# Performance work log

Measured on AMD Instinct MI355X. Metric: run time of the kernel, lower is better.

Reference implementation:

```python
import jax, jax.numpy as jnp
import numpy as np

N = 50000
IN_CH = 128
HEADS = 4
OUT_CH = 32
E = 800000
NEG_SLOPE = 0.2


def setup_inputs() -> dict:
    key = jax.random.key(0)
    k1, k2, k3, k4, k5, k6 = jax.random.split(key, 6)
    x = jax.random.normal(k1, (N, IN_CH), dtype=jnp.float32)
    edge_index = jax.random.randint(k2, (2, E), 0, N, dtype=jnp.int64)
    # learned params (PyG GATv2Conv: lin_l, lin_r weights, att vector, bias)
    s = 1.0 / np.sqrt(IN_CH)
    W_l = jax.random.uniform(k3, (IN_CH, HEADS, OUT_CH), jnp.float32, -s, s)
    W_r = jax.random.uniform(k4, (IN_CH, HEADS, OUT_CH), jnp.float32, -s, s)
    att = jax.random.uniform(k5, (HEADS, OUT_CH), jnp.float32, -s, s)
    bias = jax.random.uniform(k6, (HEADS * OUT_CH,), jnp.float32, -s, s)
    return {"x": x, "edge_index": edge_index, "W_l": W_l, "W_r": W_r,
            "att": att, "bias": bias}


def reference(x, edge_index, W_l, W_r, att, bias):
    # add self loops (PyG default add_self_loops=True)
    loops = jnp.arange(N, dtype=edge_index.dtype)
    src = jnp.concatenate([edge_index[0], loops])  # message source j
    dst = jnp.concatenate([edge_index[1], loops])  # message target i

    # node projections: [N, H, C]
    x_l = jnp.einsum('nd,dhc->nhc', x, W_l)  # source-side
    x_r = jnp.einsum('nd,dhc->nhc', x, W_r)  # target-side

    # GATv2 attention logits per edge: a^T LeakyReLU(x_l[j] + x_r[i])
    e = jax.nn.leaky_relu(x_l[src] + x_r[dst], NEG_SLOPE)  # [Etot, H, C]
    score = jnp.einsum('ehc,hc->eh', e, att)               # [Etot, H]

    # segment softmax over incoming edges of each destination node
    m = jax.ops.segment_max(score, dst, num_segments=N)    # [N, H]
    m = jnp.where(jnp.isfinite(m), m, 0.0)
    ex = jnp.exp(score - m[dst])                           # [Etot, H]
    denom = jax.ops.segment_sum(ex, dst, num_segments=N)   # [N, H]
    alpha = ex / denom[dst]                                # [Etot, H]

    # scatter-aggregate weighted messages
    msg = alpha[:, :, None] * x_l[src]                     # [Etot, H, C]
    out = jax.ops.segment_sum(msg, dst, num_segments=N)    # [N, H, C]

    # concat heads + bias
    return out.reshape(N, HEADS * OUT_CH) + bias
```

## Files before the change

kernel.cpp:

```cpp
#include <hip/hip_runtime.h>
#include <math.h>

#define N_NODES 50000
#define IN_CH   128
#define TOT_CH  128
#define NEDGE   800000
#define ETOT    (NEDGE + N_NODES)
#define MTILES  ((N_NODES + 63) / 64)
#define NBUCK   ((N_NODES + 255) / 256)
#define BCAP    8192
#define EPB     4096
#define NBIN    ((ETOT + EPB - 1) / EPB)

#define OFF_XL      ((size_t)0)
#define OFF_EBUF    ((size_t)12800000)
#define OFF_XR      ((size_t)25600000)
#define OFF_SRC     ((size_t)38400000)
#define OFF_BT      ((size_t)44900352)
#define OFF_GCUR    ((size_t)45000064)
#define OFF_ROWPTR  ((size_t)51200000)

typedef float f32x4 __attribute__((ext_vector_type(4)));
typedef short s16x8 __attribute__((ext_vector_type(8)));

__device__ __forceinline__ unsigned f2bf(float f) {
    unsigned u = __float_as_uint(f);
    return (u + 0x7fffu + ((u >> 16) & 1u)) >> 16;
}
__device__ __forceinline__ float bflo(unsigned u) { return __uint_as_float(u << 16); }
__device__ __forceinline__ float bfhi(unsigned u) { return __uint_as_float(u & 0xffff0000u); }

__device__ __forceinline__ int SWZ(int row, int byteoff) {
    return row * 256 + (byteoff ^ ((row & 7) << 4));
}

__global__ __launch_bounds__(256) void k1_kernel(
    const float* __restrict__ Wl, const float* __restrict__ Wr,
    unsigned* __restrict__ btg, const int* __restrict__ ei,
    int* __restrict__ gcur, unsigned* __restrict__ ebuf)
{
    __shared__ int lcnt[256];
    __shared__ int lbase[256];
    const int bid = blockIdx.x;
    const int tid = threadIdx.x;

    if (bid < NBIN) {
        lcnt[tid] = 0;
        __syncthreads();
        const int base = bid * EPB;
        int sv[16], dv[16];
#pragma unroll
        for (int u = 0; u < 16; ++u) {
            const int e = base + u * 256 + tid;
            int s32 = 0, d32 = -1;
            if (e < ETOT) {
                if (e < NEDGE) { s32 = ei[e]; d32 = ei[NEDGE + e]; }
                else           { s32 = d32 = e - NEDGE; }
                atomicAdd(&lcnt[d32 >> 8], 1);
            }
            sv[u] = s32; dv[u] = d32;
        }
        __syncthreads();
        if (tid < NBUCK) {
            const int v = lcnt[tid];
            lbase[tid] = v ? atomicAdd(&gcur[tid], v) : 0;
        }
        __syncthreads();
        lcnt[tid] = 0;
        __syncthreads();
#pragma unroll
        for (int u = 0; u < 16; ++u) {
            const int d32 = dv[u];
            if (d32 >= 0) {
                const int b = d32 >> 8;
                const int p = lbase[b] + atomicAdd(&lcnt[b], 1);
                ebuf[b * BCAP + p] = (unsigned)sv[u] | ((unsigned)(d32 & 255) << 16);
            }
        }
    } else {
        const int g = (bid - NBIN) * 256 + tid;
        if (g < 256 * 64) {
            const int n = g >> 6, kk = g & 63;
            const float* W = (n < 128) ? Wl : Wr;
            const int nc = n & 127;
            const float a = W[(size_t)(2 * kk) * 128 + nc];
            const float b = W[(size_t)(2 * kk + 1) * 128 + nc];
            btg[g] = f2bf(a) | (f2bf(b) << 16);
        }
    }
}

__global__ __launch_bounds__(256) void k2_kernel(
    const float* __restrict__ x, const unsigned* __restrict__ btg,
    unsigned* __restrict__ xl_bf, unsigned* __restrict__ xr_bf,
    const unsigned* __restrict__ ebuf, const int* __restrict__ gcur,
    int2* __restrict__ rowptr2, int* __restrict__ ssrc)
{
    __shared__ __align__(16) unsigned char smem[32768];
    __shared__ int wsum[4];
    const int bid = blockIdx.x;
    const int tid = threadIdx.x;

    if (bid < NBUCK) {
        int* lcnt = (int*)smem;
        int* lcur = ((int*)smem) + 256;
        const int ecnt  = gcur[bid];
        const int ebase = bid * BCAP;
        lcnt[tid] = 0;
        __syncthreads();
        for (int k = tid; k < ecnt; k += 256)
            atomicAdd(&lcnt[(ebuf[ebase + k] >> 16) & 255], 1);
        __syncthreads();
        const int lane = tid & 63, wid = tid >> 6;
        const int v = lcnt[tid];
        int s = v;
#pragma unroll
        for (int off = 1; off < 64; off <<= 1) {
            int t = __shfl_up(s, off);
            if (lane >= off) s += t;
        }
        if (lane == 63) wsum[wid] = s;
        __syncthreads();
        if (tid == 0) {
            int acc = 0;
#pragma unroll
            for (int w = 0; w < 4; ++w) { int t = wsum[w]; wsum[w] = acc; acc += t; }
        }
        __syncthreads();
        const int gpos = ebase + wsum[wid] + s - v;
        const int node = (bid << 8) + tid;
        if (node < N_NODES) rowptr2[node] = make_int2(gpos, gpos + v);
        lcur[tid] = gpos;
        __syncthreads();
        for (int k = tid; k < ecnt; k += 256) {
            const unsigned ed = ebuf[ebase + k];
            const int p = atomicAdd(&lcur[(ed >> 16) & 255], 1);
            ssrc[p] = (int)(ed & 0xffffu);
        }
        return;
    }

    unsigned char* Al = smem;
    unsigned char* Bl = smem + 16384;
    const int gb = bid - NBUCK;
    const int nt = gb / MTILES;
    const int mt = gb % MTILES;
    const int mbase = mt * 64;
    const int nbase = nt * 64;

    {
        const int r = tid >> 2, q = tid & 3;
        int gm = mbase + r;
        gm = (gm < N_NODES) ? gm : (N_NODES - 1);
        const float* xrow = x + (size_t)gm * IN_CH + q * 32;
#pragma unroll
        for (int i = 0; i < 8; ++i) {
            const float4 xv = *(const float4*)(xrow + i * 4);
            uint2 p;
            p.x = f2bf(xv.x) | (f2bf(xv.y) << 16);
            p.y = f2bf(xv.z) | (f2bf(xv.w) << 16);
            *(uint2*)(Al + SWZ(r, q * 64 + i * 8)) = p;
        }
    }
    {
        const int r = tid >> 2, q = tid & 3;
        const unsigned* brow = btg + (size_t)(nbase + r) * 64 + q * 16;
#pragma unroll
        for (int i = 0; i < 4; ++i) {
            const uint4 v = *(const uint4*)(brow + i * 4);
            *(uint4*)(Bl + SWZ(r, q * 64 + i * 16)) = v;
        }
    }
    __syncthreads();

    const int l  = tid & 63;
    const int wv = tid >> 6;

    f32x4 acc[4];
#pragma unroll
    for (int n = 0; n < 4; ++n) acc[n] = (f32x4){0.f, 0.f, 0.f, 0.f};

    s16x8 af[4];
#pragma unroll
    for (int ks = 0; ks < 4; ++ks)
        af[ks] = *(const s16x8*)(Al + SWZ(wv * 16 + (l & 15), ks * 64 + (l >> 4) * 16));

#pragma unroll
    for (int nsub = 0; nsub < 4; ++nsub) {
#pragma unroll
        for (int ks = 0; ks < 4; ++ks) {
            const s16x8 bfr = *(const s16x8*)(Bl + SWZ(nsub * 16 + (l & 15), ks * 64 + (l >> 4) * 16));
            acc[nsub] = __builtin_amdgcn_mfma_f32_16x16x32_bf16(af[ks], bfr, acc[nsub], 0, 0, 0);
        }
    }

    unsigned* dstbuf = (nt < 2) ? xl_bf : xr_bf;
    const int ncol0 = (nt & 1) * 64;
#pragma unroll
    for (int nsub = 0; nsub < 4; ++nsub) {
        const int n = ncol0 + nsub * 16 + (l & 15);
#pragma unroll
        for (int reg = 0; reg < 4; ++reg) {
            const float v  = acc[nsub][reg];
            const float vp = __shfl_xor(v, 1);
            const int row = mbase + wv * 16 + (l >> 4) * 4 + reg;
            if (((l & 1) == 0) && row < N_NODES)
                dstbuf[(size_t)row * 64 + (n >> 1)] = f2bf(v) | (f2bf(vp) << 16);
        }
    }
}

#define DPP_ADD(s, ctrl) do { \
        int _t = __builtin_amdgcn_update_dpp(0, __float_as_int(s), ctrl, 0xf, 0xf, true); \
        s += __int_as_float(_t); } while(0)

#define RED16x8(a0,a1,a2,a3,a4,a5,a6,a7) do { \
        DPP_ADD(a0,0xB1); DPP_ADD(a1,0xB1); DPP_ADD(a2,0xB1); DPP_ADD(a3,0xB1); \
        DPP_ADD(a4,0xB1); DPP_ADD(a5,0xB1); DPP_ADD(a6,0xB1); DPP_ADD(a7,0xB1); \
        DPP_ADD(a0,0x4E); DPP_ADD(a1,0x4E); DPP_ADD(a2,0x4E); DPP_ADD(a3,0x4E); \
        DPP_ADD(a4,0x4E); DPP_ADD(a5,0x4E); DPP_ADD(a6,0x4E); DPP_ADD(a7,0x4E); \
        DPP_ADD(a0,0x124); DPP_ADD(a1,0x124); DPP_ADD(a2,0x124); DPP_ADD(a3,0x124); \
        DPP_ADD(a4,0x124); DPP_ADD(a5,0x124); DPP_ADD(a6,0x124); DPP_ADD(a7,0x124); \
        DPP_ADD(a0,0x128); DPP_ADD(a1,0x128); DPP_ADD(a2,0x128); DPP_ADD(a3,0x128); \
        DPP_ADD(a4,0x128); DPP_ADD(a5,0x128); DPP_ADD(a6,0x128); DPP_ADD(a7,0x128); } while(0)

template<bool MASKED>
__device__ __forceinline__ void batch8(
    const int* __restrict__ srcs, int k, int k1, int lane,
    const unsigned* __restrict__ xl_bf,
    float xr2x, float xr2y, float a6x, float a4x, float a6y, float a4y,
    float& den, float& b0, float& b1)
{
#define KIDX(n) (MASKED ? min(k + n, k1 - 1) : (k + n))
#define LOADU(n) \
    const int j##n = __builtin_amdgcn_readfirstlane(srcs[KIDX(n)]); \
    const unsigned u##n = *(xl_bf + (size_t)j##n * 64 + lane);
    LOADU(0); LOADU(1); LOADU(2); LOADU(3);
    LOADU(4); LOADU(5); LOADU(6); LOADU(7);
#undef LOADU
#undef KIDX
#define SCORE(n) \
    const float t0_##n = bflo(u##n) + xr2x; \
    const float t1_##n = bfhi(u##n) + xr2y; \
    float s##n = fmaf(a6x, t0_##n, fmaf(a4x, fabsf(t0_##n), \
                 fmaf(a6y, t1_##n, a4y * fabsf(t1_##n))));
    SCORE(0); SCORE(1); SCORE(2); SCORE(3);
    SCORE(4); SCORE(5); SCORE(6); SCORE(7);
#undef SCORE
    RED16x8(s0, s1, s2, s3, s4, s5, s6, s7);
    if (MASKED) {
        const int r = k1 - k;
        s1 = (1 < r) ? s1 : -1e30f;
        s2 = (2 < r) ? s2 : -1e30f;
        s3 = (3 < r) ? s3 : -1e30f;
        s4 = (4 < r) ? s4 : -1e30f;
        s5 = (5 < r) ? s5 : -1e30f;
        s6 = (6 < r) ? s6 : -1e30f;
        s7 = (7 < r) ? s7 : -1e30f;
    }
    const float p0 = __builtin_amdgcn_exp2f(s0), p1 = __builtin_amdgcn_exp2f(s1);
    const float p2 = __builtin_amdgcn_exp2f(s2), p3 = __builtin_amdgcn_exp2f(s3);
    const float p4 = __builtin_amdgcn_exp2f(s4), p5 = __builtin_amdgcn_exp2f(s5);
    const float p6 = __builtin_amdgcn_exp2f(s6), p7 = __builtin_amdgcn_exp2f(s7);
    den += ((p0 + p1) + (p2 + p3)) + ((p4 + p5) + (p6 + p7));
    {
        const float e0 = fmaf(p1, t0_1, p0 * t0_0);
        const float e1 = fmaf(p3, t0_3, p2 * t0_2);
        const float e2 = fmaf(p5, t0_5, p4 * t0_4);
        const float e3 = fmaf(p7, t0_7, p6 * t0_6);
        b0 += (e0 + e1) + (e2 + e3);
        const float f0 = fmaf(p1, t1_1, p0 * t1_0);
        const float f1 = fmaf(p3, t1_3, p2 * t1_2);
        const float f2 = fmaf(p5, t1_5, p4 * t1_4);
        const float f3 = fmaf(p7, t1_7, p6 * t1_6);
        b1 += (f0 + f1) + (f2 + f3);
    }
}

__global__ __launch_bounds__(256) void gat_kernel(
    const unsigned* __restrict__ xl_bf, const unsigned* __restrict__ xr_bf,
    const int2* __restrict__ rowptr2, const int* __restrict__ srcs,
    const float* __restrict__ att, const float* __restrict__ bias,
    float* __restrict__ out)
{
    const int lane = threadIdx.x & 63;
    const int i = blockIdx.x * 4 + (threadIdx.x >> 6);
    if (i >= N_NODES) return;
    const int c = lane * 2;
    const float2 att2 = *(const float2*)(att + c);
    const unsigned ur = xr_bf[(size_t)i * 64 + lane];
    const float xr2x = bflo(ur), xr2y = bfhi(ur);
    const float LOG2E = 1.4426950408889634f;
    const float a6x = 0.6f * att2.x * LOG2E, a4x = 0.4f * att2.x * LOG2E;
    const float a6y = 0.6f * att2.y * LOG2E, a4y = 0.4f * att2.y * LOG2E;
    const int2 kr = rowptr2[i];
    const int k0 = kr.x, k1 = kr.y;

    float den = 0.f, b0 = 0.f, b1 = 0.f;
    int k = k0;
    for (; k + 8 <= k1; k += 8)
        batch8<false>(srcs, k, k1, lane, xl_bf, xr2x, xr2y,
                      a6x, a4x, a6y, a4y, den, b0, b1);
    if (k < k1)
        batch8<true>(srcs, k, k1, lane, xl_bf, xr2x, xr2y,
                     a6x, a4x, a6y, a4y, den, b0, b1);

    const float inv = 1.f / den;
    const float2 bb = *(const float2*)(bias + c);
    float2 o;
    o.x = fmaf(b0, inv, bb.x - xr2x);
    o.y = fmaf(b1, inv, bb.y - xr2y);
    *(float2*)(out + (size_t)i * TOT_CH + c) = o;
}

extern "C" void kernel_launch(void* const* d_in, const int* in_sizes, int n_in,
                              void* d_out, int out_size, void* d_ws, size_t ws_size,
                              hipStream_t stream) {
    const float* x    = (const float*)d_in[0];
    const int*   ei   = (const int*)d_in[1];
    const float* Wl   = (const float*)d_in[2];
    const float* Wr   = (const float*)d_in[3];
    const float* att  = (const float*)d_in[4];
    const float* bias = (const float*)d_in[5];
    float* out = (float*)d_out;
    char*  ws  = (char*)d_ws;

    unsigned* xl_bf = (unsigned*)(ws + OFF_XL);
    unsigned* ebuf  = (unsigned*)(ws + OFF_EBUF);
    unsigned* xr_bf = (unsigned*)(ws + OFF_XR);
    int*      ssrc  = (int*)(ws + OFF_SRC);
    unsigned* btg   = (unsigned*)(ws + OFF_BT);
    int*      gcur  = (int*)(ws + OFF_GCUR);
    int2*   rowptr2 = (int2*)(ws + OFF_ROWPTR);

    hipMemsetAsync(gcur, 0, NBUCK * sizeof(int), stream);
    hipLaunchKernelGGL(k1_kernel, dim3(NBIN + 64), dim3(256), 0, stream,
                       Wl, Wr, btg, ei, gcur, ebuf);
    hipLaunchKernelGGL(k2_kernel, dim3(NBUCK + MTILES * 4), dim3(256), 0, stream,
                       x, btg, xl_bf, xr_bf, ebuf, gcur, rowptr2, ssrc);
    hipLaunchKernelGGL(gat_kernel, dim3((N_NODES + 3) / 4), dim3(256), 0, stream,
                       xl_bf, xr_bf, rowptr2, ssrc, att, bias, out);
}
```

Baseline: 91.81 us.

## Reuse x tile across all four weight column tiles in projection GEMM

Each GEMM block now loads and converts its 64-row x tile to bf16 once, then loops over the four 64-column weight tiles (covering both x_l and x_r), reloading only the B tile between iterations. This cuts the grid from four times MTILES to MTILES GEMM blocks and removes three redundant fp32 loads and conversions of x per row tile. The cost is fewer, longer blocks with extra barriers per weight tile. Separately, the row-pointer bounds in the attention kernel are made wave-uniform with readfirstlane so the loop control can stay in scalar registers.

```diff
diff --git a/kernel.cpp b/kernel.cpp
--- a/kernel.cpp
+++ b/kernel.cpp
@@ -142,11 +142,10 @@
 
     unsigned char* Al = smem;
     unsigned char* Bl = smem + 16384;
-    const int gb = bid - NBUCK;
-    const int nt = gb / MTILES;
-    const int mt = gb % MTILES;
+    const int mt = bid - NBUCK;
     const int mbase = mt * 64;
-    const int nbase = nt * 64;
+    const int l  = tid & 63;
+    const int wv = tid >> 6;
 
     {
         const int r = tid >> 2, q = tid & 3;
@@ -164,7 +163,7 @@
     }
     {
         const int r = tid >> 2, q = tid & 3;
-        const unsigned* brow = btg + (size_t)(nbase + r) * 64 + q * 16;
+        const unsigned* brow = btg + (size_t)r * 64 + q * 16;
 #pragma unroll
         for (int i = 0; i < 4; ++i) {
             const uint4 v = *(const uint4*)(brow + i * 4);
@@ -173,40 +172,49 @@
     }
     __syncthreads();
 
-    const int l  = tid & 63;
-    const int wv = tid >> 6;
-
-    f32x4 acc[4];
-#pragma unroll
-    for (int n = 0; n < 4; ++n) acc[n] = (f32x4){0.f, 0.f, 0.f, 0.f};
-
     s16x8 af[4];
 #pragma unroll
     for (int ks = 0; ks < 4; ++ks)
         af[ks] = *(const s16x8*)(Al + SWZ(wv * 16 + (l & 15), ks * 64 + (l >> 4) * 16));
 
-#pragma unroll
-    for (int nsub = 0; nsub < 4; ++nsub) {
-#pragma unroll
-        for (int ks = 0; ks < 4; ++ks) {
-            const s16x8 bfr = *(const s16x8*)(Bl + SWZ(nsub * 16 + (l & 15), ks * 64 + (l >> 4) * 16));
-            acc[nsub] = __builtin_amdgcn_mfma_f32_16x16x32_bf16(af[ks], bfr, acc[nsub], 0, 0, 0);
-        }
-    }
-
-    unsigned* dstbuf = (nt < 2) ? xl_bf : xr_bf;
-    const int ncol0 = (nt & 1) * 64;
-#pragma unroll
-    for (int nsub = 0; nsub < 4; ++nsub) {
-        const int n = ncol0 + nsub * 16 + (l & 15);
-#pragma unroll
-        for (int reg = 0; reg < 4; ++reg) {
-            const float v  = acc[nsub][reg];
-            const float vp = __shfl_xor(v, 1);
-            const int row = mbase + wv * 16 + (l >> 4) * 4 + reg;
-            if (((l & 1) == 0) && row < N_NODES)
-                dstbuf[(size_t)row * 64 + (n >> 1)] = f2bf(v) | (f2bf(vp) << 16);
-        }
+    for (int nt4 = 0; nt4 < 4; ++nt4) {
+        f32x4 acc[4];
+#pragma unroll
+        for (int n = 0; n < 4; ++n) acc[n] = (f32x4){0.f, 0.f, 0.f, 0.f};
+#pragma unroll
+        for (int nsub = 0; nsub < 4; ++nsub) {
+#pragma unroll
+            for (int ks = 0; ks < 4; ++ks) {
+                const s16x8 bfr = *(const s16x8*)(Bl + SWZ(nsub * 16 + (l & 15), ks * 64 + (l >> 4) * 16));
+                acc[nsub] = __builtin_amdgcn_mfma_f32_16x16x32_bf16(af[ks], bfr, acc[nsub], 0, 0, 0);
+            }
+        }
+        unsigned* dstbuf = (nt4 < 2) ? xl_bf : xr_bf;
+        const int ncol0 = (nt4 & 1) * 64;
+#pragma unroll
+        for (int nsub = 0; nsub < 4; ++nsub) {
+            const int n = ncol0 + nsub * 16 + (l & 15);
+#pragma unroll
+            for (int reg = 0; reg < 4; ++reg) {
+                const float v  = acc[nsub][reg];
+                const float vp = __shfl_xor(v, 1);
+                const int row = mbase + wv * 16 + (l >> 4) * 4 + reg;
+                if (((l & 1) == 0) && row < N_NODES)
+                    dstbuf[(size_t)row * 64 + (n >> 1)] = f2bf(v) | (f2bf(vp) << 16);
+            }
+        }
+        if (nt4 == 3) break;
+        __syncthreads();
+        {
+            const int r = tid >> 2, q = tid & 3;
+            const unsigned* brow = btg + (size_t)((nt4 + 1) * 64 + r) * 64 + q * 16;
+#pragma unroll
+            for (int i = 0; i < 4; ++i) {
+                const uint4 v = *(const uint4*)(brow + i * 4);
+                *(uint4*)(Bl + SWZ(r, q * 64 + i * 16)) = v;
+            }
+        }
+        __syncthreads();
     }
 }
 
@@ -294,7 +302,8 @@
     const float a6x = 0.6f * att2.x * LOG2E, a4x = 0.4f * att2.x * LOG2E;
     const float a6y = 0.6f * att2.y * LOG2E, a4y = 0.4f * att2.y * LOG2E;
     const int2 kr = rowptr2[i];
-    const int k0 = kr.x, k1 = kr.y;
+    const int k0 = __builtin_amdgcn_readfirstlane(kr.x);
+    const int k1 = __builtin_amdgcn_readfirstlane(kr.y);
 
     float den = 0.f, b0 = 0.f, b1 = 0.f;
     int k = k0;
@@ -336,7 +345,7 @@
     hipMemsetAsync(gcur, 0, NBUCK * sizeof(int), stream);
     hipLaunchKernelGGL(k1_kernel, dim3(NBIN + 64), dim3(256), 0, stream,
                        Wl, Wr, btg, ei, gcur, ebuf);
-    hipLaunchKernelGGL(k2_kernel, dim3(NBUCK + MTILES * 4), dim3(256), 0, stream,
+    hipLaunchKernelGGL(k2_kernel, dim3(NBUCK + MTILES), dim3(256), 0, stream,
                        x, btg, xl_bf, xr_bf, ebuf, gcur, rowptr2, ssrc);
     hipLaunchKernelGGL(gat_kernel, dim3((N_NODES + 3) / 4), dim3(256), 0, stream,
                        xl_bf, xr_bf, rowptr2, ssrc, att, bias, out);
```

New measurement: 78.42 us, median of 2. -14.6%, faster.
